# Kernel optimization log

Hardware: AMD Instinct MI355X
Metric: run time of the kernel (lower is better)

The kernel has to match this reference:

```python
import jax, jax.numpy as jnp
import numpy as np
import jax.scipy.linalg as jsl

# dims
B, DIN = 4096, 256      # data
OUT, M = 32, 128        # output GPs, inducing points
NH = 2                  # hyperparameter samples
JITTER = 1e-4


def vec2tril(vec, m):
    """Fill lower-triangular (row-major) from packed vector."""
    i, j = jnp.tril_indices(m)
    out = jnp.zeros(vec.shape[:-1] + (m, m), vec.dtype)
    return out.at[..., i, j].set(vec)


def _hypers(theta):
    sf2 = jnp.exp(theta[:, 0])        # (NH,) signal variance
    ls = jnp.exp(theta[:, 1:])        # (NH, DIN) ARD lengthscales
    return sf2, ls


def kernel_zz(theta, z):
    """RBF K(z,z): (NH, OUT, M, M)."""
    sf2, ls = _hypers(theta)
    zs = z[None] / ls[:, None, None, :]              # (NH, OUT, M, DIN)
    n2 = (zs ** 2).sum(-1)                           # (NH, OUT, M)
    cross = jnp.einsum('homd,hond->homn', zs, zs)
    d2 = jnp.maximum(n2[..., :, None] + n2[..., None, :] - 2.0 * cross, 0.0)
    return sf2[:, None, None, None] * jnp.exp(-0.5 * d2)


def kernel_zx(theta, z, x):
    """RBF K(z,x): (NH, OUT, M, B)."""
    sf2, ls = _hypers(theta)
    zs = z[None] / ls[:, None, None, :]              # (NH, OUT, M, DIN)
    xs = x[None] / ls[:, None, :]                    # (NH, B, DIN)
    z2 = (zs ** 2).sum(-1)                           # (NH, OUT, M)
    x2 = (xs ** 2).sum(-1)                           # (NH, B)
    cross = jnp.einsum('homd,hbd->homb', zs, xs)     # (NH, OUT, M, B)
    d2 = jnp.maximum(z2[..., None] + x2[:, None, None, :] - 2.0 * cross, 0.0)
    return sf2[:, None, None, None] * jnp.exp(-0.5 * d2)


def setup_inputs() -> dict:
    key = jax.random.key(0)
    k1, k2, k3, k4, k5 = jax.random.split(key, 5)
    x = jax.random.normal(k1, (B, DIN), jnp.float32)
    z = jax.random.normal(k2, (OUT, M, DIN), jnp.float32)
    u_mean = jax.random.normal(k3, (OUT, M, 1), jnp.float32) * 0.5
    u_tril_vec = jax.random.uniform(k4, (OUT, M * (M + 1) // 2), jnp.float32)
    theta = jax.random.normal(k5, (NH, 1 + DIN), jnp.float32)
    return {"x": x, "z": z, "u_mean": u_mean, "u_tril_vec": u_tril_vec, "theta": theta}


def reference(x, z, u_mean, u_tril_vec, theta):
    m = z.shape[-2]
    u_tril = vec2tril(u_tril_vec, m)                        # (OUT, M, M)

    kuf = kernel_zx(theta, z, x)                            # (NH, OUT, M, B)
    kuu = kernel_zz(theta, z)                               # (NH, OUT, M, M)
    Lkuu = jnp.linalg.cholesky(kuu + JITTER * jnp.eye(m, dtype=kuu.dtype))

    bshape = Lkuu.shape[:-2]
    u_mean_b = jnp.broadcast_to(u_mean, bshape + u_mean.shape[-2:])
    u_tril_b = jnp.broadcast_to(u_tril, bshape + u_tril.shape[-2:])

    LKinvu = jsl.solve_triangular(Lkuu, u_mean_b, lower=True)   # (NH, OUT, M, 1)
    LKinvKuf = jsl.solve_triangular(Lkuu, kuf, lower=True)      # (NH, OUT, M, B)

    sf2, _ = _hypers(theta)
    kff_diag = sf2[:, None, None]                               # (NH, 1, 1)

    diag1 = (LKinvKuf ** 2).sum(-2)                             # (NH, OUT, B)
    LKinvLs = jsl.solve_triangular(Lkuu, u_tril_b, lower=True)  # (NH, OUT, M, M)
    vec2 = jnp.einsum('...ij,...ik->...jk', LKinvLs, LKinvKuf)  # (NH, OUT, M, B)
    diag2 = (vec2 ** 2).sum(-2)                                 # (NH, OUT, B)

    mu = jnp.einsum('...ij,...ik->...jk', LKinvKuf, LKinvu)[..., 0]  # (NH, OUT, B)
    var = kff_diag - diag1 + diag2                                   # (NH, OUT, B)
    return mu, var
```

## Files before the change

### kernel.cpp

```cpp
#include <hip/hip_runtime.h>
#include <cstdint>
#include <cstddef>

constexpr int B_   = 4096;
constexpr int DIN  = 256;
constexpr int OUT_ = 32;
constexpr int MM   = 128;
constexpr int NH_  = 2;
constexpr int HO   = 64;
constexpr int TRIL = 8256;
constexpr float JIT = 1e-4f;

constexpr size_t al4k(size_t x){ return (x + 4095) & ~size_t(4095); }
constexpr size_t OFF_FLAG  = 0;
constexpr size_t OFF_INVLS = 4096;
constexpr size_t OFF_SF2   = al4k(OFF_INVLS + 2*256*4);
constexpr size_t OFF_ZN2   = al4k(OFF_SF2 + 64);
constexpr size_t OFF_XN2   = al4k(OFF_ZN2 + 8192*4);
constexpr size_t OFF_W     = al4k(OFF_XN2 + 8192*4);
constexpr size_t OFF_ZS    = al4k(OFF_W + 8192*4);
constexpr size_t OFF_XS    = al4k(OFF_ZS + (size_t)2097152*2);
constexpr size_t OFF_VTH   = al4k(OFF_XS + (size_t)2097152*2);
constexpr size_t OFF_VTL   = al4k(OFF_VTH + (size_t)1048576*2);
constexpr size_t OFF_CHI   = al4k(OFF_VTL + (size_t)1048576*2);
constexpr size_t OFF_CLO   = al4k(OFF_CHI + (size_t)1048576*2);

typedef float f32x4 __attribute__((ext_vector_type(4)));
typedef short short8 __attribute__((ext_vector_type(8)));

__device__ __forceinline__ float bf2f(unsigned short u){
  union{unsigned int i; float f;} v; v.i = ((unsigned)u) << 16; return v.f;
}
__device__ __forceinline__ unsigned short f2bf(float f){
  union{float f; unsigned int i;} v; v.f = f;
  unsigned int r = v.i + 0x7fffu + ((v.i >> 16) & 1u);
  return (unsigned short)(r >> 16);
}
__device__ __forceinline__ float ldin(const void* p, size_t i, int isbf){
  if (isbf) return bf2f(((const unsigned short*)p)[i]);
  return ((const float*)p)[i];
}
__device__ __forceinline__ void stout(void* p, size_t i, float v, int isbf){
  if (isbf) ((unsigned short*)p)[i] = f2bf(v);
  else ((float*)p)[i] = v;
}
__device__ __forceinline__ void gl_lds16(const unsigned short* g, unsigned short* l){
  __builtin_amdgcn_global_load_lds(
      (const __attribute__((address_space(1))) unsigned int*)g,
      (__attribute__((address_space(3))) unsigned int*)l, 16, 0, 0);
}

__global__ void k_hypers(const void* __restrict__ theta, const void* __restrict__ x,
                         int* __restrict__ flagp,
                         float* __restrict__ inv_ls, float* __restrict__ sf2){
  __shared__ int sflag;
  int t = threadIdx.x;
  if (t < 64){
    unsigned int w0 = ((const unsigned int*)theta)[t];
    unsigned int w1 = ((const unsigned int*)x)[t];
    float a0 = fabsf(bf2f((unsigned short)(w0 & 0xffffu)));
    float a1 = fabsf(bf2f((unsigned short)(w1 & 0xffffu)));
    int c = ((a0 > 9.3e-10f && a0 < 64.f) ? 1 : 0) + ((a1 > 9.3e-10f && a1 < 64.f) ? 1 : 0);
    c += __shfl_down(c, 32); c += __shfl_down(c, 16); c += __shfl_down(c, 8);
    c += __shfl_down(c, 4);  c += __shfl_down(c, 2);  c += __shfl_down(c, 1);
    if (t == 0){ sflag = (c >= 64) ? 1 : 0; *flagp = sflag; }
  }
  __syncthreads();
  const int isbf = sflag;
  for (int i = t; i < NH_*257; i += blockDim.x){
    int h = i / 257, j = i - h*257;
    float v = ldin(theta, i, isbf);
    if (j == 0) sf2[h] = __expf(v);
    else inv_ls[h*DIN + j - 1] = __expf(-v);
  }
}

__global__ void k_scale(const void* __restrict__ xsrc, const void* __restrict__ zsrc,
                        const int* flagp, const float* __restrict__ inv_ls,
                        unsigned short* __restrict__ xdst, unsigned short* __restrict__ zdst,
                        float* __restrict__ xn2, float* __restrict__ zn2){
  const int isbf = *flagp;
  const int wave = threadIdx.x >> 6, lane = threadIdx.x & 63;
  int bx = blockIdx.x;
  const void* src; unsigned short* dst; float* n2; int r;
  if (bx < 1024){ src = xsrc; dst = xdst; n2 = xn2; r = bx*4 + wave; }
  else          { src = zsrc; dst = zdst; n2 = zn2; r = (bx-1024)*4 + wave; }
  const int d0 = lane*4;
  float v[4];
  if (isbf){
    uint2 uu = *(const uint2*)((const unsigned short*)src + (size_t)r*DIN + d0);
    v[0]=bf2f((unsigned short)(uu.x & 0xffffu)); v[1]=bf2f((unsigned short)(uu.x >> 16));
    v[2]=bf2f((unsigned short)(uu.y & 0xffffu)); v[3]=bf2f((unsigned short)(uu.y >> 16));
  } else {
    f32x4 f = *(const f32x4*)((const float*)src + (size_t)r*DIN + d0);
    v[0]=f[0]; v[1]=f[1]; v[2]=f[2]; v[3]=f[3];
  }
  #pragma unroll
  for (int h = 0; h < 2; ++h){
    f32x4 il = *(const f32x4*)(inv_ls + h*DIN + d0);
    unsigned short rb[4];
    float p = 0.f;
    #pragma unroll
    for (int k = 0; k < 4; ++k){
      float s = v[k] * il[k];
      rb[k] = f2bf(s);
      float qv = bf2f(rb[k]);
      p += qv*qv;
    }
    uint2 pk;
    pk.x = (unsigned)rb[0] | ((unsigned)rb[1] << 16);
    pk.y = (unsigned)rb[2] | ((unsigned)rb[3] << 16);
    *(uint2*)(dst + ((size_t)h*4096 + r)*DIN + d0) = pk;
    p += __shfl_xor(p, 32); p += __shfl_xor(p, 16); p += __shfl_xor(p, 8);
    p += __shfl_xor(p, 4);  p += __shfl_xor(p, 2);  p += __shfl_xor(p, 1);
    if (lane == 0) n2[(size_t)h*4096 + r] = p;
  }
}

constexpr int TLD = 20;
constexpr int TSZ = 16*TLD;
__device__ __forceinline__ int tb(int bi, int bj){ return (bi*(bi+1)/2 + bj)*TSZ; }
__device__ __forceinline__ int vb(int bi, int bj){ return (36 + bi*(bi-1)/2 + bj)*TSZ; }
__device__ __forceinline__ int tri_bi(int t){
  int bi = (int)((sqrtf(8.f*t + 1.f) - 1.f) * 0.5f);
  while ((bi+1)*(bi+2)/2 <= t) ++bi;
  while (bi*(bi+1)/2 > t) --bi;
  return bi;
}

__global__ __launch_bounds__(512) void k_kufact(
    const unsigned short* __restrict__ zs, const float* __restrict__ zn2,
    const float* __restrict__ sf2,
    unsigned short* __restrict__ VTh, unsigned short* __restrict__ VTl){
  const int ho = blockIdx.x, h = ho >> 5;
  const int tid = threadIdx.x;
  const int lane = tid & 63, wid = tid >> 6;
  const int l15 = lane & 15, q = lane >> 4;
  const int wn = wid * 16;
  extern __shared__ float T[];
  unsigned short* zsl = (unsigned short*)T;
  float* zn2l = T + 64*TSZ;
  if (tid < 128) zn2l[tid] = zn2[ho*128 + tid];
  const size_t zbase = (size_t)ho * 32768;
  const int sw = ((q ^ ((l15 >> 1) & 3)) << 3);
  const int rA = wn + (lane >> 2);
  const int sg = ((lane & 3) ^ ((rA >> 1) & 3)) << 3;
  const f32x4 z4 = {0.f,0.f,0.f,0.f};
  f32x4 acc[8];
  #pragma unroll
  for (int mt=0; mt<8; ++mt) acc[mt]=z4;
  for (int kc = 0; kc < 8; ++kc){
    __syncthreads();
    gl_lds16(zs + zbase + (size_t)rA*256 + kc*32 + sg, zsl + wn*32);
    __syncthreads();
    short8 b0 = *(const short8*)(zsl + (wn + l15)*32 + sw);
    #pragma unroll
    for (int mt=0; mt<8; ++mt){
      short8 a = *(const short8*)(zsl + (mt*16 + l15)*32 + sw);
      acc[mt] = __builtin_amdgcn_mfma_f32_16x16x32_bf16(a, b0, acc[mt], 0,0,0);
    }
  }
  __syncthreads();
  const float s2v = sf2[h];
  {
    const int n = wn + l15;
    const float nn = zn2l[n];
    const int bn = wid;
    #pragma unroll
    for (int mt=0; mt<8; ++mt){
      #pragma unroll
      for (int r=0; r<4; ++r){
        int m = mt*16 + q*4 + r;
        float d2 = fmaxf(zn2l[m] + nn - 2.f*acc[mt][r], 0.f);
        float a = s2v * __expf(-0.5f*d2);
        if (m == n) a += JIT;
        int bm = m >> 4;
        if (bn <= bm) T[tb(bm, bn) + (m & 15)*TLD + (n & 15)] = a;
      }
    }
  }
  __syncthreads();
  for (int kb = 0; kb < 8; ++kb){
    if (wid == 0){
      float* D = T + tb(kb, kb);
      const int r = lane & 15;
      const bool act = (lane < 16);
      float a[16];
      #pragma unroll
      for (int k = 0; k < 16; ++k) a[k] = 0.f;
      if (act){
        #pragma unroll
        for (int k2 = 0; k2 < 4; ++k2)
          *(f32x4*)(a + 4*k2) = *(const f32x4*)(D + r*TLD + 4*k2);
      }
      #pragma unroll
      for (int c = 0; c < 16; ++c){
        float pr[16];
        #pragma unroll
        for (int k = 0; k < 16; ++k) pr[k] = __shfl(a[k], c);
        float rsq = rsqrtf(pr[c]);
        if (act && r >= c) a[c] *= rsq;
        float lrc = a[c];
        #pragma unroll
        for (int k = 0; k < 16; ++k)
          if (k > c && act && r > c) a[k] -= lrc * (pr[k] * rsq);
      }
      float v[16];
      #pragma unroll
      for (int k = 0; k < 16; ++k) v[k] = 0.f;
      const int c = lane & 15;
      #pragma unroll
      for (int i = 0; i < 16; ++i){
        float lrow[16];
        #pragma unroll
        for (int k = 0; k < 16; ++k) lrow[k] = __shfl(a[k], i);
        float rli = 1.f / lrow[i];
        float s = 0.f;
        #pragma unroll
        for (int k = 0; k < 16; ++k)
          if (k < i) s += ((k >= c) ? lrow[k]*v[k] : 0.f);
        v[i] = (c == i) ? rli : ((c < i) ? -s*rli : 0.f);
      }
      if (act){
        #pragma unroll
        for (int i = 0; i < 16; ++i) D[i*TLD + c] = v[i];
      }
    }
    __syncthreads();
    {
      const int gi = kb*16 + 16 + tid;
      if (gi < 128){
        float* Bp = T + tb(gi >> 4, kb) + (gi & 15)*TLD;
        const float* Vd = T + tb(kb, kb);
        float b[16], nb[16];
        #pragma unroll
        for (int k2 = 0; k2 < 4; ++k2) *(f32x4*)(b + 4*k2) = *(const f32x4*)(Bp + 4*k2);
        #pragma unroll
        for (int j = 0; j < 16; ++j){
          float s = 0.f;
          #pragma unroll
          for (int k = 0; k < 16; ++k)
            if (k <= j) s += b[k] * Vd[j*TLD + k];
          nb[j] = s;
        }
        #pragma unroll
        for (int k2 = 0; k2 < 4; ++k2) *(f32x4*)(Bp + 4*k2) = *(const f32x4*)(nb + 4*k2);
      }
    }
    __syncthreads();
    {
      const int D8 = 7 - kb;
      const int Tn = D8*(D8+1)/2;
      const int r15 = lane & 15, c0 = (lane >> 4)*4;
      for (int tt = wid; tt < Tn; tt += 8){
        int bi1 = tri_bi(tt);
        int bj1 = tt - bi1*(bi1+1)/2;
        int bi = kb + 1 + bi1, bj = kb + 1 + bj1;
        const float* Lr = T + tb(bi, kb) + r15*TLD;
        const float* Lc = T + tb(bj, kb) + c0*TLD;
        float* Cp = T + tb(bi, bj) + r15*TLD + c0;
        float lr[16];
        #pragma unroll
        for (int k2 = 0; k2 < 4; ++k2) *(f32x4*)(lr + 4*k2) = *(const f32x4*)(Lr + 4*k2);
        f32x4 accv = *(const f32x4*)Cp;
        #pragma unroll
        for (int cc = 0; cc < 4; ++cc){
          float lc[16];
          #pragma unroll
          for (int k2 = 0; k2 < 4; ++k2) *(f32x4*)(lc + 4*k2) = *(const f32x4*)(Lc + cc*TLD + 4*k2);
          float s = 0.f;
          #pragma unroll
          for (int k = 0; k < 16; ++k) s += lr[k]*lc[k];
          accv[cc] -= s;
        }
        *(f32x4*)Cp = accv;
      }
    }
    __syncthreads();
  }
  {
    const int r15 = lane & 15, c0 = (lane >> 4)*4;
    for (int d = 1; d < 8; ++d){
      for (int tt = wid; tt < 8 - d; tt += 8){
        const int bi = d + tt, jb = bi - d;
        float W0=0.f, W1=0.f, W2=0.f, W3=0.f;
        for (int k = jb; k < bi; ++k){
          const float* Lt = T + tb(bi, k) + r15*TLD;
          const float* Vt = (k == jb) ? (T + tb(jb, jb)) : (T + vb(k, jb));
          float lr[16];
          #pragma unroll
          for (int k2 = 0; k2 < 4; ++k2) *(f32x4*)(lr + 4*k2) = *(const f32x4*)(Lt + 4*k2);
          #pragma unroll
          for (int kk = 0; kk < 16; ++kk){
            f32x4 vv = *(const f32x4*)(Vt + kk*TLD + c0);
            W0 += lr[kk]*vv[0]; W1 += lr[kk]*vv[1];
            W2 += lr[kk]*vv[2]; W3 += lr[kk]*vv[3];
          }
        }
        const float* Vd = T + tb(bi, bi) + r15*TLD;
        const int cgl = (lane >> 4);
        f32x4 Rr = {0.f,0.f,0.f,0.f};
        #pragma unroll
        for (int k = 0; k < 16; ++k){
          float vd = Vd[k];
          float w0 = __shfl(W0, (cgl<<4)|k);
          float w1 = __shfl(W1, (cgl<<4)|k);
          float w2 = __shfl(W2, (cgl<<4)|k);
          float w3 = __shfl(W3, (cgl<<4)|k);
          Rr[0] -= vd*w0; Rr[1] -= vd*w1; Rr[2] -= vd*w2; Rr[3] -= vd*w3;
        }
        *(f32x4*)(T + vb(bi, jb) + r15*TLD + c0) = Rr;
      }
      __syncthreads();
    }
  }
  const size_t obase = (size_t)ho * 16384;
  for (int e = tid; e < 16384; e += 512){
    int c = e >> 7, rr = e & 127;
    int bc = c >> 4, br = rr >> 4;
    float v = 0.f;
    if (br == bc)      v = T[tb(br, bc) + (rr & 15)*TLD + (c & 15)];
    else if (br > bc)  v = T[vb(br, bc) + (rr & 15)*TLD + (c & 15)];
    unsigned short hi = f2bf(v);
    unsigned short lo = f2bf(v - bf2f(hi));
    VTh[obase + e] = hi;
    VTl[obase + e] = lo;
  }
}

__global__ __launch_bounds__(512) void k_QPC(
    const unsigned short* __restrict__ VTh, const unsigned short* __restrict__ VTl,
    const void* __restrict__ u_mean, const void* __restrict__ u_tril, const int* flagp,
    float* __restrict__ wg, unsigned short* __restrict__ Chi,
    unsigned short* __restrict__ Clo){
  const int ho = blockIdx.x, o = ho & 31;
  const int tid = threadIdx.x;
  const int lane = tid & 63, l15 = lane & 15, q = lane >> 4;
  const int wid = tid >> 6;
  const int wn = wid * 16;
  const int isbf = *flagp;
  extern __shared__ char smem[];
  unsigned short* Qh  = (unsigned short*)smem;
  unsigned short* Ql  = (unsigned short*)(smem + 34816);
  unsigned short* Sth = (unsigned short*)(smem + 69632);
  unsigned short* Stl = (unsigned short*)(smem + 104448);
  float* ul    = (float*)(smem + 139264);
  float* wpart = ul + 128;
  unsigned short* hsl = Qh;
  unsigned short* lsl = Qh + 4096;
  if (tid < 128) ul[tid] = ldin(u_mean, (size_t)o*128 + tid, isbf);
  for (int e = tid; e < 16384; e += 512){
    int k = e >> 7, j = e & 127;
    float val = 0.f;
    if (j <= k) val = ldin(u_tril, (size_t)o*TRIL + (size_t)k*(k+1)/2 + j, isbf);
    unsigned short hi = f2bf(val);
    Sth[j*136 + k] = hi;
    Stl[j*136 + k] = f2bf(val - bf2f(hi));
  }
  const size_t vbase = (size_t)ho * 16384;
  const int sw = ((q ^ ((l15 >> 1) & 3)) << 3);
  const int rA = wn + (lane >> 2);
  const int sg = ((lane & 3) ^ ((rA >> 1) & 3)) << 3;
  const f32x4 z4 = {0.f,0.f,0.f,0.f};
  f32x4 acc[8];
  #pragma unroll
  for (int mt=0; mt<8; ++mt) acc[mt]=z4;
  for (int kc = 0; kc < 4; ++kc){
    __syncthreads();
    gl_lds16(VTh + vbase + (size_t)rA*128 + kc*32 + sg, hsl + wn*32);
    gl_lds16(VTl + vbase + (size_t)rA*128 + kc*32 + sg, lsl + wn*32);
    __syncthreads();
    short8 b0h = *(const short8*)(hsl + (wn + l15)*32 + sw);
    short8 b0l = *(const short8*)(lsl + (wn + l15)*32 + sw);
    #pragma unroll
    for (int mt=0; mt<8; ++mt){
      short8 ah = *(const short8*)(hsl + (mt*16 + l15)*32 + sw);
      short8 al = *(const short8*)(lsl + (mt*16 + l15)*32 + sw);
      acc[mt] = __builtin_amdgcn_mfma_f32_16x16x32_bf16(ah, b0h, acc[mt], 0,0,0);
      acc[mt] = __builtin_amdgcn_mfma_f32_16x16x32_bf16(ah, b0l, acc[mt], 0,0,0);
      acc[mt] = __builtin_amdgcn_mfma_f32_16x16x32_bf16(al, b0h, acc[mt], 0,0,0);
    }
  }
  {
    float u0 = ul[wn + l15];
    float wpm[32];
    #pragma unroll
    for (int mt=0; mt<8; ++mt){
      #pragma unroll
      for (int r=0; r<4; ++r)
        wpm[mt*4+r] = acc[mt][r]*u0;
    }
    #pragma unroll
    for (int i = 0; i < 32; ++i){
      wpm[i] += __shfl_xor(wpm[i], 1);
      wpm[i] += __shfl_xor(wpm[i], 2);
      wpm[i] += __shfl_xor(wpm[i], 4);
      wpm[i] += __shfl_xor(wpm[i], 8);
    }
    if (l15 == 0){
      #pragma unroll
      for (int i = 0; i < 32; ++i){
        int m = (i>>2)*16 + q*4 + (i&3);
        wpart[wid*128 + m] = wpm[i];
      }
    }
  }
  __syncthreads();
  if (tid < 128){
    float s = 0.f;
    #pragma unroll
    for (int wv = 0; wv < 8; ++wv) s += wpart[wv*128 + tid];
    wg[ho*128 + tid] = s;
  }
  {
    const int n0 = wn + l15;
    #pragma unroll
    for (int mt=0; mt<8; ++mt){
      #pragma unroll
      for (int r=0; r<4; ++r){
        int m = mt*16 + q*4 + r;
        float v0 = acc[mt][r];
        unsigned short h0 = f2bf(v0);
        Qh[m*136 + n0] = h0; Ql[m*136 + n0] = f2bf(v0 - bf2f(h0));
      }
    }
  }
  __syncthreads();
  f32x4 acc3[8];
  #pragma unroll
  for (int mt=0; mt<8; ++mt) acc3[mt]=z4;
  #pragma unroll
  for (int kc2 = 0; kc2 < 4; ++kc2){
    const int ko = kc2*32 + q*8;
    short8 b0h = *(const short8*)(Sth + (wn + l15)*136 + ko);
    short8 b0l = *(const short8*)(Stl + (wn + l15)*136 + ko);
    #pragma unroll
    for (int mt=0; mt<8; ++mt){
      short8 ah = *(const short8*)(Qh + (mt*16 + l15)*136 + ko);
      short8 al = *(const short8*)(Ql + (mt*16 + l15)*136 + ko);
      acc3[mt] = __builtin_amdgcn_mfma_f32_16x16x32_bf16(ah, b0h, acc3[mt], 0,0,0);
      acc3[mt] = __builtin_amdgcn_mfma_f32_16x16x32_bf16(al, b0h, acc3[mt], 0,0,0);
      acc3[mt] = __builtin_amdgcn_mfma_f32_16x16x32_bf16(ah, b0l, acc3[mt], 0,0,0);
    }
  }
  __syncthreads();
  {
    unsigned short* Ph = Qh;
    unsigned short* Pl = Ql;
    const int n0 = wn + l15;
    #pragma unroll
    for (int mt=0; mt<8; ++mt){
      #pragma unroll
      for (int r=0; r<4; ++r){
        int m = mt*16 + q*4 + r;
        float v0 = acc3[mt][r];
        unsigned short h0 = f2bf(v0);
        Ph[m*136 + n0] = h0; Pl[m*136 + n0] = f2bf(v0 - bf2f(h0));
      }
    }
  }
  __syncthreads();
  f32x4 acc2[8];
  #pragma unroll
  for (int mt=0; mt<8; ++mt) acc2[mt]=z4;
  #pragma unroll
  for (int kc2 = 0; kc2 < 4; ++kc2){
    const int ko = kc2*32 + q*8;
    short8 b0h = *(const short8*)(Qh + (wn + l15)*136 + ko);
    short8 b0l = *(const short8*)(Ql + (wn + l15)*136 + ko);
    #pragma unroll
    for (int mt=0; mt<8; ++mt){
      short8 ah = *(const short8*)(Qh + (mt*16 + l15)*136 + ko);
      short8 al = *(const short8*)(Ql + (mt*16 + l15)*136 + ko);
      acc2[mt] = __builtin_amdgcn_mfma_f32_16x16x32_bf16(ah, b0h, acc2[mt], 0,0,0);
      acc2[mt] = __builtin_amdgcn_mfma_f32_16x16x32_bf16(ah, b0l, acc2[mt], 0,0,0);
      acc2[mt] = __builtin_amdgcn_mfma_f32_16x16x32_bf16(al, b0h, acc2[mt], 0,0,0);
    }
  }
  {
    const int n = wn + l15;
    #pragma unroll
    for (int mt=0; mt<8; ++mt){
      #pragma unroll
      for (int r=0; r<4; ++r){
        int m = mt*16 + q*4 + r;
        float c = acc[mt][r] - acc2[mt][r];
        unsigned short hi = f2bf(c);
        unsigned short lo = f2bf(c - bf2f(hi));
        Chi[vbase + m*128 + n] = hi;
        Clo[vbase + m*128 + n] = lo;
      }
    }
  }
}

__global__ __launch_bounds__(256, 2) void k_main(
    const unsigned short* __restrict__ zs, const unsigned short* __restrict__ xs,
    const float* __restrict__ zn2, const float* __restrict__ xn2,
    const float* __restrict__ wg, const unsigned short* __restrict__ Chi,
    const unsigned short* __restrict__ Clo, const float* __restrict__ sf2,
    const int* flagp, void* __restrict__ out){
  const int bblk = blockIdx.x, ho = blockIdx.y, h = ho >> 5;
  const int tid = threadIdx.x;
  const int lane = tid & 63, l15 = lane & 15, q = lane >> 4;
  const int wid = tid >> 6;
  const int wn = wid * 32;
  const int wn2 = wid * 64;
  const int isbf = *flagp;
  extern __shared__ char smem[];
  unsigned short* zb0 = (unsigned short*)smem;
  unsigned short* zb1 = zb0 + 4096;
  unsigned short* zb2 = zb0 + 8192;
  unsigned short* kufT = (unsigned short*)smem;
  float* zn2l = (float*)(smem + 69632);
  float* xn2l = zn2l + 128;
  float* wl   = xn2l + 256;

  if (tid < 128){
    zn2l[tid] = zn2[ho*128 + tid];
    wl[tid]   = wg[ho*128 + tid];
  }
  xn2l[tid] = xn2[(size_t)h*B_ + bblk*256 + tid];
  const size_t zbase = (size_t)ho * 32768;
  const size_t xbase = ((size_t)h*B_ + bblk*256) * 256;
  const int sw = ((q ^ ((l15 >> 1) & 3)) << 3);
  const int rA = wn + (lane >> 2);
  const int sg = ((lane & 3) ^ ((rA >> 1) & 3)) << 3;
  const f32x4 z4 = {0.f,0.f,0.f,0.f};
  f32x4 acc[8][4];
  #pragma unroll
  for (int mt=0; mt<8; ++mt){
    #pragma unroll
    for (int nt=0; nt<4; ++nt) acc[mt][nt]=z4;
  }
  unsigned short* zbp[3] = { zb0, zb1, zb2 };

  auto STAGEZ = [&](int c, unsigned short* zd){
    const int off = c*32;
    gl_lds16(zs + zbase + (size_t)rA*256      + off + sg, zd + wn*32);
    gl_lds16(zs + zbase + (size_t)(rA+16)*256 + off + sg, zd + (wn+16)*32);
  };
  auto LDB = [&](int c, short8* bd){
    #pragma unroll
    for (int nt=0; nt<4; ++nt)
      bd[nt] = *(const short8*)(xs + xbase + (size_t)(wn2 + nt*16 + l15)*256 + c*32 + q*8);
  };

  short8 bA[4], bB[4];
  STAGEZ(0, zb0);
  STAGEZ(1, zb1);
  LDB(0, bA);

  #pragma unroll
  for (int kc = 0; kc < 8; ++kc){
    unsigned short* zc = zbp[kc % 3];
    if (kc + 2 < 8) STAGEZ(kc + 2, zbp[(kc + 2) % 3]);
    if (kc + 1 < 8){ if (kc & 1) LDB(kc + 1, bA); else LDB(kc + 1, bB); }
    if (kc < 6)       asm volatile("s_waitcnt vmcnt(6)" ::: "memory");
    else if (kc == 6) asm volatile("s_waitcnt vmcnt(4)" ::: "memory");
    else              asm volatile("s_waitcnt vmcnt(0)" ::: "memory");
    __builtin_amdgcn_s_barrier();
    __builtin_amdgcn_sched_barrier(0);
    const short8* bc = (kc & 1) ? bB : bA;
    #pragma unroll
    for (int mt=0; mt<8; ++mt){
      short8 a = *(const short8*)(zc + (mt*16 + l15)*32 + sw);
      #pragma unroll
      for (int nt=0; nt<4; ++nt)
        acc[mt][nt] = __builtin_amdgcn_mfma_f32_16x16x32_bf16(a, bc[nt], acc[mt][nt], 0,0,0);
    }
    asm volatile("s_waitcnt lgkmcnt(0)" ::: "memory");
    __builtin_amdgcn_sched_barrier(0);
    __builtin_amdgcn_s_barrier();
  }
  const float s2 = sf2[h];
  float mu[4] = {0.f, 0.f, 0.f, 0.f};
  #pragma unroll
  for (int nt=0; nt<4; ++nt){
    const int bl = wn2 + nt*16 + l15;
    const float xn = xn2l[bl];
    #pragma unroll
    for (int mt=0; mt<8; ++mt){
      const int m0 = mt*16 + q*4;
      float kf[4];
      #pragma unroll
      for (int r=0; r<4; ++r){
        float d2 = fmaxf(zn2l[m0+r] + xn - 2.f*acc[mt][nt][r], 0.f);
        kf[r] = s2 * __expf(-0.5f*d2);
        mu[nt] += wl[m0+r] * kf[r];
      }
      uint2 pk;
      pk.x = (unsigned)f2bf(kf[0]) | ((unsigned)f2bf(kf[1]) << 16);
      pk.y = (unsigned)f2bf(kf[2]) | ((unsigned)f2bf(kf[3]) << 16);
      *(uint2*)(kufT + (size_t)bl*136 + m0) = pk;
    }
  }
  __syncthreads();
  f32x4 acc2[8][4];
  #pragma unroll
  for (int mt=0; mt<8; ++mt){
    #pragma unroll
    for (int nt=0; nt<4; ++nt) acc2[mt][nt]=z4;
  }
  const unsigned short* Ch = Chi + (size_t)ho*16384;
  const unsigned short* Cl = Clo + (size_t)ho*16384;
  #pragma unroll
  for (int kc2 = 0; kc2 < 4; ++kc2){
    short8 bk[4];
    #pragma unroll
    for (int nt=0; nt<4; ++nt)
      bk[nt] = *(const short8*)(kufT + (wn2 + nt*16 + l15)*136 + kc2*32 + q*8);
    #pragma unroll
    for (int mt=0; mt<8; ++mt){
      short8 ah = *(const short8*)(Ch + (mt*16 + l15)*128 + kc2*32 + q*8);
      short8 al = *(const short8*)(Cl + (mt*16 + l15)*128 + kc2*32 + q*8);
      #pragma unroll
      for (int nt=0; nt<4; ++nt){
        acc2[mt][nt] = __builtin_amdgcn_mfma_f32_16x16x32_bf16(ah, bk[nt], acc2[mt][nt], 0,0,0);
        acc2[mt][nt] = __builtin_amdgcn_mfma_f32_16x16x32_bf16(al, bk[nt], acc2[mt][nt], 0,0,0);
      }
    }
  }
  float s2p[4] = {0.f, 0.f, 0.f, 0.f};
  #pragma unroll
  for (int nt=0; nt<4; ++nt){
    const int bl = wn2 + nt*16 + l15;
    #pragma unroll
    for (int mt=0; mt<8; ++mt){
      const int m0 = mt*16 + q*4;
      uint2 pk = *(const uint2*)(kufT + (size_t)bl*136 + m0);
      f32x4 t = acc2[mt][nt];
      s2p[nt] += bf2f((unsigned short)(pk.x & 0xffff)) * t[0]
               + bf2f((unsigned short)(pk.x >> 16))    * t[1]
               + bf2f((unsigned short)(pk.y & 0xffff)) * t[2]
               + bf2f((unsigned short)(pk.y >> 16))    * t[3];
    }
  }
  #pragma unroll
  for (int nt=0; nt<4; ++nt){
    mu[nt]  += __shfl_xor(mu[nt], 16);  mu[nt]  += __shfl_xor(mu[nt], 32);
    s2p[nt] += __shfl_xor(s2p[nt], 16); s2p[nt] += __shfl_xor(s2p[nt], 32);
  }
  if (lane < 16){
    #pragma unroll
    for (int nt=0; nt<4; ++nt){
      size_t col = (size_t)ho*B_ + bblk*256 + wn2 + nt*16 + lane;
      stout(out, col,                  mu[nt],        isbf);
      stout(out, (size_t)HO*B_ + col,  s2 - s2p[nt],  isbf);
    }
  }
}

extern "C" void kernel_launch(void* const* d_in, const int* in_sizes, int n_in,
                              void* d_out, int out_size, void* d_ws, size_t ws_size,
                              hipStream_t stream) {
  const void* x      = d_in[0];
  const void* z      = d_in[1];
  const void* u_mean = d_in[2];
  const void* u_tril = d_in[3];
  const void* theta  = d_in[4];
  char* ws = (char*)d_ws;

  int*   flag   = (int*)(ws + OFF_FLAG);
  float* inv_ls = (float*)(ws + OFF_INVLS);
  float* sf2    = (float*)(ws + OFF_SF2);
  float* zn2    = (float*)(ws + OFF_ZN2);
  float* xn2    = (float*)(ws + OFF_XN2);
  float* wv     = (float*)(ws + OFF_W);
  unsigned short* zsw = (unsigned short*)(ws + OFF_ZS);
  unsigned short* xsw = (unsigned short*)(ws + OFF_XS);
  unsigned short* VTh = (unsigned short*)(ws + OFF_VTH);
  unsigned short* VTl = (unsigned short*)(ws + OFF_VTL);
  unsigned short* Chi = (unsigned short*)(ws + OFF_CHI);
  unsigned short* Clo = (unsigned short*)(ws + OFF_CLO);

  k_hypers<<<1, 256, 0, stream>>>(theta, x, flag, inv_ls, sf2);
  k_scale<<<dim3(2048), 256, 0, stream>>>(x, z, flag, inv_ls, xsw, zsw, xn2, zn2);
  k_kufact<<<64, 512, (64*TSZ + 128) * 4, stream>>>(zsw, zn2, sf2, VTh, VTl);
  k_QPC<<<64, 512, 139264 + 512 + 4096, stream>>>(VTh, VTl, u_mean, u_tril, flag, wv, Chi, Clo);
  k_main<<<dim3(16, 64), 256, 69632 + 2048, stream>>>(zsw, xsw, zn2, xn2, wv, Chi, Clo, sf2, flag, (void*)d_out);
}
```

Measured before the change: 226.0 us.

## Fuse Cholesky-factor kernel with QPC kernel, keeping VT in LDS

Merges k_kufact and k_QPC into one k_fact kernel per (h,o) block. The inverse-factor VT now stays in shared memory with a padded layout and is never written to or reloaded from global memory. This removes one kernel launch and the global round trip. It raises per-block LDS to about 153 KB and relies on careful aliasing of the shared buffers across phases.

```diff
diff --git a/kernel.cpp b/kernel.cpp
--- a/kernel.cpp
+++ b/kernel.cpp
@@ -128,27 +128,43 @@
   return bi;
 }
 
-__global__ __launch_bounds__(512) void k_kufact(
+__global__ __launch_bounds__(512) void k_fact(
     const unsigned short* __restrict__ zs, const float* __restrict__ zn2,
     const float* __restrict__ sf2,
-    unsigned short* __restrict__ VTh, unsigned short* __restrict__ VTl){
-  const int ho = blockIdx.x, h = ho >> 5;
+    const void* __restrict__ u_mean, const void* __restrict__ u_tril,
+    const int* flagp, float* __restrict__ wg,
+    unsigned short* __restrict__ Chi, unsigned short* __restrict__ Clo){
+  const int ho = blockIdx.x, h = ho >> 5, o = ho & 31;
   const int tid = threadIdx.x;
   const int lane = tid & 63, wid = tid >> 6;
   const int l15 = lane & 15, q = lane >> 4;
   const int wn = wid * 16;
-  extern __shared__ float T[];
+  const int isbf = *flagp;
+  extern __shared__ char smem[];
+  float* T = (float*)smem;
+  float* zn2l = T + 64*TSZ;
   unsigned short* zsl = (unsigned short*)T;
-  float* zn2l = T + 64*TSZ;
-  if (tid < 128) zn2l[tid] = zn2[ho*128 + tid];
+  unsigned short* VTh = (unsigned short*)(smem + 82432);
+  unsigned short* VTl = (unsigned short*)(smem + 117248);
+  unsigned short* Sth = (unsigned short*)smem;
+  unsigned short* Stl = (unsigned short*)(smem + 34816);
+  unsigned short* Qh = VTh;
+  unsigned short* Ql = VTl;
+  float* ul    = (float*)(smem + 152064);
+  float* wpart = (float*)(smem + 152576);
+
+  if (tid < 128){
+    zn2l[tid] = zn2[ho*128 + tid];
+    ul[tid]   = ldin(u_mean, (size_t)o*128 + tid, isbf);
+  }
   const size_t zbase = (size_t)ho * 32768;
   const int sw = ((q ^ ((l15 >> 1) & 3)) << 3);
   const int rA = wn + (lane >> 2);
   const int sg = ((lane & 3) ^ ((rA >> 1) & 3)) << 3;
   const f32x4 z4 = {0.f,0.f,0.f,0.f};
-  f32x4 acc[8];
-  #pragma unroll
-  for (int mt=0; mt<8; ++mt) acc[mt]=z4;
+  f32x4 acck[8];
+  #pragma unroll
+  for (int mt=0; mt<8; ++mt) acck[mt]=z4;
   for (int kc = 0; kc < 8; ++kc){
     __syncthreads();
     gl_lds16(zs + zbase + (size_t)rA*256 + kc*32 + sg, zsl + wn*32);
@@ -157,7 +173,7 @@
     #pragma unroll
     for (int mt=0; mt<8; ++mt){
       short8 a = *(const short8*)(zsl + (mt*16 + l15)*32 + sw);
-      acc[mt] = __builtin_amdgcn_mfma_f32_16x16x32_bf16(a, b0, acc[mt], 0,0,0);
+      acck[mt] = __builtin_amdgcn_mfma_f32_16x16x32_bf16(a, b0, acck[mt], 0,0,0);
     }
   }
   __syncthreads();
@@ -171,7 +187,7 @@
       #pragma unroll
       for (int r=0; r<4; ++r){
         int m = mt*16 + q*4 + r;
-        float d2 = fmaxf(zn2l[m] + nn - 2.f*acc[mt][r], 0.f);
+        float d2 = fmaxf(zn2l[m] + nn - 2.f*acck[mt][r], 0.f);
         float a = s2v * __expf(-0.5f*d2);
         if (m == n) a += JIT;
         int bm = m >> 4;
@@ -314,7 +330,6 @@
       __syncthreads();
     }
   }
-  const size_t obase = (size_t)ho * 16384;
   for (int e = tid; e < 16384; e += 512){
     int c = e >> 7, rr = e & 127;
     int bc = c >> 4, br = rr >> 4;
@@ -322,33 +337,71 @@
     if (br == bc)      v = T[tb(br, bc) + (rr & 15)*TLD + (c & 15)];
     else if (br > bc)  v = T[vb(br, bc) + (rr & 15)*TLD + (c & 15)];
     unsigned short hi = f2bf(v);
-    unsigned short lo = f2bf(v - bf2f(hi));
-    VTh[obase + e] = hi;
-    VTl[obase + e] = lo;
-  }
-}
-
-__global__ __launch_bounds__(512) void k_QPC(
-    const unsigned short* __restrict__ VTh, const unsigned short* __restrict__ VTl,
-    const void* __restrict__ u_mean, const void* __restrict__ u_tril, const int* flagp,
-    float* __restrict__ wg, unsigned short* __restrict__ Chi,
-    unsigned short* __restrict__ Clo){
-  const int ho = blockIdx.x, o = ho & 31;
-  const int tid = threadIdx.x;
-  const int lane = tid & 63, l15 = lane & 15, q = lane >> 4;
-  const int wid = tid >> 6;
-  const int wn = wid * 16;
-  const int isbf = *flagp;
-  extern __shared__ char smem[];
-  unsigned short* Qh  = (unsigned short*)smem;
-  unsigned short* Ql  = (unsigned short*)(smem + 34816);
-  unsigned short* Sth = (unsigned short*)(smem + 69632);
-  unsigned short* Stl = (unsigned short*)(smem + 104448);
-  float* ul    = (float*)(smem + 139264);
-  float* wpart = ul + 128;
-  unsigned short* hsl = Qh;
-  unsigned short* lsl = Qh + 4096;
-  if (tid < 128) ul[tid] = ldin(u_mean, (size_t)o*128 + tid, isbf);
+    VTh[c*136 + rr] = hi;
+    VTl[c*136 + rr] = f2bf(v - bf2f(hi));
+  }
+  __syncthreads();
+  f32x4 acc[8];
+  #pragma unroll
+  for (int mt=0; mt<8; ++mt) acc[mt]=z4;
+  #pragma unroll
+  for (int kc2 = 0; kc2 < 4; ++kc2){
+    const int ko = kc2*32 + q*8;
+    short8 b0h = *(const short8*)(VTh + (wn + l15)*136 + ko);
+    short8 b0l = *(const short8*)(VTl + (wn + l15)*136 + ko);
+    #pragma unroll
+    for (int mt=0; mt<8; ++mt){
+      short8 ah = *(const short8*)(VTh + (mt*16 + l15)*136 + ko);
+      short8 al = *(const short8*)(VTl + (mt*16 + l15)*136 + ko);
+      acc[mt] = __builtin_amdgcn_mfma_f32_16x16x32_bf16(ah, b0h, acc[mt], 0,0,0);
+      acc[mt] = __builtin_amdgcn_mfma_f32_16x16x32_bf16(ah, b0l, acc[mt], 0,0,0);
+      acc[mt] = __builtin_amdgcn_mfma_f32_16x16x32_bf16(al, b0h, acc[mt], 0,0,0);
+    }
+  }
+  {
+    float u0 = ul[wn + l15];
+    float wpm[32];
+    #pragma unroll
+    for (int mt=0; mt<8; ++mt){
+      #pragma unroll
+      for (int r=0; r<4; ++r)
+        wpm[mt*4+r] = acc[mt][r]*u0;
+    }
+    #pragma unroll
+    for (int i = 0; i < 32; ++i){
+      wpm[i] += __shfl_xor(wpm[i], 1);
+      wpm[i] += __shfl_xor(wpm[i], 2);
+      wpm[i] += __shfl_xor(wpm[i], 4);
+      wpm[i] += __shfl_xor(wpm[i], 8);
+    }
+    if (l15 == 0){
+      #pragma unroll
+      for (int i = 0; i < 32; ++i){
+        int m = (i>>2)*16 + q*4 + (i&3);
+        wpart[wid*128 + m] = wpm[i];
+      }
+    }
+  }
+  __syncthreads();
+  if (tid < 128){
+    float s = 0.f;
+    #pragma unroll
+    for (int wv = 0; wv < 8; ++wv) s += wpart[wv*128 + tid];
+    wg[ho*128 + tid] = s;
+  }
+  {
+    const int n0 = wn + l15;
+    #pragma unroll
+    for (int mt=0; mt<8; ++mt){
+      #pragma unroll
+      for (int r=0; r<4; ++r){
+        int m = mt*16 + q*4 + r;
+        float v0 = acc[mt][r];
+        unsigned short h0 = f2bf(v0);
+        Qh[m*136 + n0] = h0; Ql[m*136 + n0] = f2bf(v0 - bf2f(h0));
+      }
+    }
+  }
   for (int e = tid; e < 16384; e += 512){
     int k = e >> 7, j = e & 127;
     float val = 0.f;
@@ -357,74 +410,6 @@
     Sth[j*136 + k] = hi;
     Stl[j*136 + k] = f2bf(val - bf2f(hi));
   }
-  const size_t vbase = (size_t)ho * 16384;
-  const int sw = ((q ^ ((l15 >> 1) & 3)) << 3);
-  const int rA = wn + (lane >> 2);
-  const int sg = ((lane & 3) ^ ((rA >> 1) & 3)) << 3;
-  const f32x4 z4 = {0.f,0.f,0.f,0.f};
-  f32x4 acc[8];
-  #pragma unroll
-  for (int mt=0; mt<8; ++mt) acc[mt]=z4;
-  for (int kc = 0; kc < 4; ++kc){
-    __syncthreads();
-    gl_lds16(VTh + vbase + (size_t)rA*128 + kc*32 + sg, hsl + wn*32);
-    gl_lds16(VTl + vbase + (size_t)rA*128 + kc*32 + sg, lsl + wn*32);
-    __syncthreads();
-    short8 b0h = *(const short8*)(hsl + (wn + l15)*32 + sw);
-    short8 b0l = *(const short8*)(lsl + (wn + l15)*32 + sw);
-    #pragma unroll
-    for (int mt=0; mt<8; ++mt){
-      short8 ah = *(const short8*)(hsl + (mt*16 + l15)*32 + sw);
-      short8 al = *(const short8*)(lsl + (mt*16 + l15)*32 + sw);
-      acc[mt] = __builtin_amdgcn_mfma_f32_16x16x32_bf16(ah, b0h, acc[mt], 0,0,0);
-      acc[mt] = __builtin_amdgcn_mfma_f32_16x16x32_bf16(ah, b0l, acc[mt], 0,0,0);
-      acc[mt] = __builtin_amdgcn_mfma_f32_16x16x32_bf16(al, b0h, acc[mt], 0,0,0);
-    }
-  }
-  {
-    float u0 = ul[wn + l15];
-    float wpm[32];
-    #pragma unroll
-    for (int mt=0; mt<8; ++mt){
-      #pragma unroll
-      for (int r=0; r<4; ++r)
-        wpm[mt*4+r] = acc[mt][r]*u0;
-    }
-    #pragma unroll
-    for (int i = 0; i < 32; ++i){
-      wpm[i] += __shfl_xor(wpm[i], 1);
-      wpm[i] += __shfl_xor(wpm[i], 2);
-      wpm[i] += __shfl_xor(wpm[i], 4);
-      wpm[i] += __shfl_xor(wpm[i], 8);
-    }
-    if (l15 == 0){
-      #pragma unroll
-      for (int i = 0; i < 32; ++i){
-        int m = (i>>2)*16 + q*4 + (i&3);
-        wpart[wid*128 + m] = wpm[i];
-      }
-    }
-  }
-  __syncthreads();
-  if (tid < 128){
-    float s = 0.f;
-    #pragma unroll
-    for (int wv = 0; wv < 8; ++wv) s += wpart[wv*128 + tid];
-    wg[ho*128 + tid] = s;
-  }
-  {
-    const int n0 = wn + l15;
-    #pragma unroll
-    for (int mt=0; mt<8; ++mt){
-      #pragma unroll
-      for (int r=0; r<4; ++r){
-        int m = mt*16 + q*4 + r;
-        float v0 = acc[mt][r];
-        unsigned short h0 = f2bf(v0);
-        Qh[m*136 + n0] = h0; Ql[m*136 + n0] = f2bf(v0 - bf2f(h0));
-      }
-    }
-  }
   __syncthreads();
   f32x4 acc3[8];
   #pragma unroll
@@ -445,8 +430,6 @@
   }
   __syncthreads();
   {
-    unsigned short* Ph = Qh;
-    unsigned short* Pl = Ql;
     const int n0 = wn + l15;
     #pragma unroll
     for (int mt=0; mt<8; ++mt){
@@ -455,7 +438,7 @@
         int m = mt*16 + q*4 + r;
         float v0 = acc3[mt][r];
         unsigned short h0 = f2bf(v0);
-        Ph[m*136 + n0] = h0; Pl[m*136 + n0] = f2bf(v0 - bf2f(h0));
+        Qh[m*136 + n0] = h0; Ql[m*136 + n0] = f2bf(v0 - bf2f(h0));
       }
     }
   }
@@ -478,6 +461,7 @@
     }
   }
   {
+    const size_t vbase = (size_t)ho * 16384;
     const int n = wn + l15;
     #pragma unroll
     for (int mt=0; mt<8; ++mt){
@@ -669,14 +653,11 @@
   float* wv     = (float*)(ws + OFF_W);
   unsigned short* zsw = (unsigned short*)(ws + OFF_ZS);
   unsigned short* xsw = (unsigned short*)(ws + OFF_XS);
-  unsigned short* VTh = (unsigned short*)(ws + OFF_VTH);
-  unsigned short* VTl = (unsigned short*)(ws + OFF_VTL);
   unsigned short* Chi = (unsigned short*)(ws + OFF_CHI);
   unsigned short* Clo = (unsigned short*)(ws + OFF_CLO);
 
   k_hypers<<<1, 256, 0, stream>>>(theta, x, flag, inv_ls, sf2);
   k_scale<<<dim3(2048), 256, 0, stream>>>(x, z, flag, inv_ls, xsw, zsw, xn2, zn2);
-  k_kufact<<<64, 512, (64*TSZ + 128) * 4, stream>>>(zsw, zn2, sf2, VTh, VTl);
-  k_QPC<<<64, 512, 139264 + 512 + 4096, stream>>>(VTh, VTl, u_mean, u_tril, flag, wv, Chi, Clo);
+  k_fact<<<64, 512, 156672, stream>>>(zsw, zn2, sf2, u_mean, u_tril, flag, wv, Chi, Clo);
   k_main<<<dim3(16, 64), 256, 69632 + 2048, stream>>>(zsw, xsw, zn2, xn2, wv, Chi, Clo, sf2, flag, (void*)d_out);
 }
```

Result: no change. 226.1 us, median of 2 (+0.1%).
